# Performance work log

Measured on AMD Instinct MI355X. Metric: run time of the kernel, lower is better.

The kernel has to match this reference:

```python
import jax, jax.numpy as jnp
import numpy as np

B, L, D = 4, 4096, 256
INIT_ALPHA = -2.0
INV_TEMP = 1.0 / 0.1


def setup_inputs() -> dict:
    key = jax.random.key(0)
    k1, k2, k3, k4 = jax.random.split(key, 4)
    latents = jax.random.normal(k1, (B, L, D), dtype=jnp.float32)
    current_coords = jax.random.normal(k2, (B, L, 2), dtype=jnp.float32)
    # Linear(D, D, bias=False) weights (torch stores [out, in]; y = x @ W.T)
    lim = 1.0 / np.sqrt(D)
    Wq = jax.random.uniform(k3, (D, D), minval=-lim, maxval=lim, dtype=jnp.float32)
    Wk = jax.random.uniform(k4, (D, D), minval=-lim, maxval=lim, dtype=jnp.float32)
    alpha_raw = jnp.asarray(INIT_ALPHA, dtype=jnp.float32)
    return {"latents": latents, "current_coords": current_coords,
            "Wq": Wq, "Wk": Wk, "alpha_raw": alpha_raw, "layer_idx": 3}


def _l2norm(x, eps=1e-12):
    # F.normalize(dim=-1): x / max(||x||, eps)
    n = jnp.sqrt(jnp.sum(x * x, axis=-1, keepdims=True))
    return x / jnp.maximum(n, eps)


def reference(latents, current_coords, Wq, Wk, alpha_raw, layer_idx):
    # pred_idx selection (share_weights=True): 0 if layer_idx==0 else 1;
    # layer_idx=3 -> params given are for pred_idx=1.
    q = _l2norm(jnp.einsum('bld,ed->ble', latents, Wq))  # [B,L,D]
    k = _l2norm(jnp.einsum('bld,ed->ble', latents, Wk))  # [B,L,D]
    scores = jnp.einsum('bld,bmd->blm', q, k) * INV_TEMP  # [B,L,L]
    scores = jnp.clip(scores, -50.0, 50.0)
    W = jax.nn.softmax(scores, axis=-1)                   # [B,L,L]
    alpha = jax.nn.sigmoid(alpha_raw)
    # M = alpha*W + (1-alpha)*I; M @ coords == alpha*(W@coords) + (1-alpha)*coords
    new_coords = alpha * jnp.einsum('blm,bmc->blc', W, current_coords) \
                 + (1.0 - alpha) * current_coords
    displacement = new_coords - current_coords
    return (new_coords, displacement)
```

## Files before the change

### kernel.cpp

```cpp
#include <hip/hip_runtime.h>
#include <hip/hip_bf16.h>

#define BB 4
#define LL 4096
#define DD 256
#define MM (BB * LL)
#define NSPLIT 8
#define NQB (LL / 128)
#define KPS (LL / NSPLIT)
#define KT 64

typedef short short8 __attribute__((ext_vector_type(8)));
typedef float floatx4 __attribute__((ext_vector_type(4)));

#define SCALE_LOG2E 14.426950408889634f

__device__ __forceinline__ unsigned short f2bf(float f) {
    __hip_bfloat16 h = __float2bfloat16(f);
    union { __hip_bfloat16 h; unsigned short s; } c; c.h = h; return c.s;
}

__device__ __forceinline__ float fast_exp2(float x) {
#if __has_builtin(__builtin_amdgcn_exp2f)
    return __builtin_amdgcn_exp2f(x);
#else
    return exp2f(x);
#endif
}

__device__ __forceinline__ void stage16(const char* g, char* l, int lane) {
#if __has_builtin(__builtin_amdgcn_global_load_lds)
    __builtin_amdgcn_global_load_lds(
        (const __attribute__((address_space(1))) void*)(g + lane * 16),
        (__attribute__((address_space(3))) void*)l, 16, 0, 0);
#else
    *(short8*)(l + lane * 16) = *(const short8*)(g + lane * 16);
#endif
}

__global__ __launch_bounds__(256) void cvt_swz_kernel(
    const float* __restrict__ src, unsigned short* __restrict__ dst)
{
    const int t = blockIdx.x * 256 + threadIdx.x;
    const int r = t >> 5, c = t & 31;
    const float4 v0 = ((const float4*)src)[t * 2];
    const float4 v1 = ((const float4*)src)[t * 2 + 1];
    short8 o;
    o[0] = (short)f2bf(v0.x); o[1] = (short)f2bf(v0.y);
    o[2] = (short)f2bf(v0.z); o[3] = (short)f2bf(v0.w);
    o[4] = (short)f2bf(v1.x); o[5] = (short)f2bf(v1.y);
    o[6] = (short)f2bf(v1.z); o[7] = (short)f2bf(v1.w);
    const int cs = c ^ (r & 7);
    *(short8*)(dst + (size_t)r * DD + cs * 8) = o;
}

__global__ __launch_bounds__(256) void proj_norm_kernel(
    const float* __restrict__ latents,
    const __hip_bfloat16* __restrict__ Wq,
    const __hip_bfloat16* __restrict__ Wk,
    __hip_bfloat16* __restrict__ qn,
    __hip_bfloat16* __restrict__ kn)
{
    __shared__ char lds[KT * 512];

    const int tid  = threadIdx.x;
    const int wave = tid >> 6;
    const int lane = tid & 63;
    const int n15  = lane & 15;
    const int quad = lane >> 4;
    const int sw   = n15 & 7;

    const int pass = blockIdx.x & 1;
    const int rb   = blockIdx.x >> 1;
    const int m0   = rb * 64 + wave * 16;

    short8 afrag[8];
    const float* Abase = latents + (size_t)(m0 + n15) * DD + quad * 8;
#pragma unroll
    for (int kk = 0; kk < 8; ++kk) {
        const float4 v0 = *(const float4*)(Abase + kk * 32);
        const float4 v1 = *(const float4*)(Abase + kk * 32 + 4);
        short8 f;
        f[0] = (short)f2bf(v0.x); f[1] = (short)f2bf(v0.y);
        f[2] = (short)f2bf(v0.z); f[3] = (short)f2bf(v0.w);
        f[4] = (short)f2bf(v1.x); f[5] = (short)f2bf(v1.y);
        f[6] = (short)f2bf(v1.z); f[7] = (short)f2bf(v1.w);
        afrag[kk] = f;
    }

    const char* W = (const char*)(pass ? Wk : Wq);

    floatx4 acc[16];
#pragma unroll
    for (int ct = 0; ct < 16; ++ct) acc[ct] = (floatx4){0.f, 0.f, 0.f, 0.f};

    for (int round = 0; round < 4; ++round) {
        const char* src = W + (size_t)round * 32768 + wave * 8192;
        char* ldst = lds + wave * 8192;
#pragma unroll
        for (int j = 0; j < 8; ++j)
            stage16(src + j * 1024, ldst + j * 1024, lane);
        __syncthreads();

#pragma unroll
        for (int jt = 0; jt < 4; ++jt) {
            const int ct = round * 4 + jt;
            const char* lbase = lds + (jt * 16 + n15) * 512;
            floatx4 a = acc[ct];
#pragma unroll
            for (int kk = 0; kk < 8; ++kk) {
                const int chunk = (4 * kk + quad) ^ sw;
                short8 bfr = *(const short8*)(lbase + chunk * 16);
                a = __builtin_amdgcn_mfma_f32_16x16x32_bf16(afrag[kk], bfr, a, 0, 0, 0);
            }
            acc[ct] = a;
        }
        __syncthreads();
    }

    float ss[4] = {0.f, 0.f, 0.f, 0.f};
#pragma unroll
    for (int ct = 0; ct < 16; ++ct)
#pragma unroll
        for (int r = 0; r < 4; ++r) ss[r] += acc[ct][r] * acc[ct][r];
#pragma unroll
    for (int r = 0; r < 4; ++r) {
        ss[r] += __shfl_xor(ss[r], 1, 64);
        ss[r] += __shfl_xor(ss[r], 2, 64);
        ss[r] += __shfl_xor(ss[r], 4, 64);
        ss[r] += __shfl_xor(ss[r], 8, 64);
    }
    float sc[4];
#pragma unroll
    for (int r = 0; r < 4; ++r) {
        sc[r] = 1.f / fmaxf(sqrtf(ss[r]), 1e-12f);
        if (pass == 0) sc[r] *= SCALE_LOG2E;
    }

    if (pass == 0) {
#pragma unroll
        for (int ct = 0; ct < 16; ++ct) {
            const int col = ct * 16 + n15;
            const size_t base = (size_t)(m0 + quad * 4) * DD + col;
#pragma unroll
            for (int r = 0; r < 4; ++r)
                qn[base + (size_t)r * DD] = __float2bfloat16(acc[ct][r] * sc[r]);
        }
    } else {
#pragma unroll
        for (int ct = 0; ct < 16; ++ct) {
            const int col = ct * 16 + n15;
            const int c  = col >> 3, w8 = col & 7;
#pragma unroll
            for (int r = 0; r < 4; ++r) {
                const int row = m0 + quad * 4 + r;
                const int cs = c ^ (row & 7);
                kn[(size_t)row * DD + cs * 8 + w8] = __float2bfloat16(acc[ct][r] * sc[r]);
            }
        }
    }
}

__global__ __launch_bounds__(256) void attn_kernel(
    const __hip_bfloat16* __restrict__ qn,
    const __hip_bfloat16* __restrict__ kn,
    const float* __restrict__ coords,
    float* __restrict__ partials)
{
    __shared__ char lds[KT * 512];

    const int tid  = threadIdx.x;
    const int wave = tid >> 6;
    const int lane = tid & 63;
    const int n15  = lane & 15;
    const int quad = lane >> 4;
    const int sw   = n15 & 7;

    int bs = blockIdx.x;
    const int qb    = bs % NQB;    bs /= NQB;
    const int split = bs % NSPLIT; bs /= NSPLIT;
    const int b     = bs;

    const int mw = b * LL + qb * 128 + wave * 32;

    short8 aq[2][8];
#pragma unroll
    for (int rt = 0; rt < 2; ++rt) {
        const short* Qbase = (const short*)qn + (size_t)(mw + rt * 16 + n15) * DD + quad * 8;
#pragma unroll
        for (int kk = 0; kk < 8; ++kk)
            aq[rt][kk] = *(const short8*)(Qbase + kk * 32);
    }

    float s0[2][4], s1[2][4], s2[2][4];
#pragma unroll
    for (int rt = 0; rt < 2; ++rt)
#pragma unroll
        for (int r = 0; r < 4; ++r) { s0[rt][r] = 0.f; s1[rt][r] = 0.f; s2[rt][r] = 0.f; }

    const int key_base = b * LL + split * KPS;
    const char* ksrc = (const char*)kn + (size_t)key_base * 512;

    for (int kt = 0; kt < KPS / KT; ++kt) {
        const char* src = ksrc + (size_t)kt * KT * 512 + wave * 8192;
        char* ldst = lds + wave * 8192;
#pragma unroll
        for (int j = 0; j < 8; ++j)
            stage16(src + j * 1024, ldst + j * 1024, lane);
        __syncthreads();

#pragma unroll
        for (int ct = 0; ct < 4; ++ct) {
            const int kidx = key_base + kt * KT + ct * 16 + n15;
            const float2 cc = *(const float2*)(coords + (size_t)kidx * 2);

            floatx4 acc0 = (floatx4){0.f, 0.f, 0.f, 0.f};
            floatx4 acc1 = (floatx4){0.f, 0.f, 0.f, 0.f};
            const char* lbase = lds + (ct * 16 + n15) * 512;
#pragma unroll
            for (int kk = 0; kk < 8; ++kk) {
                const int chunk = (4 * kk + quad) ^ sw;
                short8 bfr = *(const short8*)(lbase + chunk * 16);
                acc0 = __builtin_amdgcn_mfma_f32_16x16x32_bf16(aq[0][kk], bfr, acc0, 0, 0, 0);
                acc1 = __builtin_amdgcn_mfma_f32_16x16x32_bf16(aq[1][kk], bfr, acc1, 0, 0, 0);
            }
#pragma unroll
            for (int r = 0; r < 4; ++r) {
                const float e0 = fast_exp2(acc0[r]);
                const float e1 = fast_exp2(acc1[r]);
                s0[0][r] += e0;
                s1[0][r] = fmaf(cc.x, e0, s1[0][r]);
                s2[0][r] = fmaf(cc.y, e0, s2[0][r]);
                s0[1][r] += e1;
                s1[1][r] = fmaf(cc.x, e1, s1[1][r]);
                s2[1][r] = fmaf(cc.y, e1, s2[1][r]);
            }
        }
        __syncthreads();
    }

#pragma unroll
    for (int rt = 0; rt < 2; ++rt)
#pragma unroll
        for (int r = 0; r < 4; ++r)
#pragma unroll
            for (int mask = 1; mask <= 8; mask <<= 1) {
                s0[rt][r] += __shfl_xor(s0[rt][r], mask, 64);
                s1[rt][r] += __shfl_xor(s1[rt][r], mask, 64);
                s2[rt][r] += __shfl_xor(s2[rt][r], mask, 64);
            }

    if (n15 == 0) {
#pragma unroll
        for (int rt = 0; rt < 2; ++rt)
#pragma unroll
            for (int r = 0; r < 4; ++r) {
                const int m = mw + rt * 16 + quad * 4 + r;
                float* p = partials + ((size_t)split * MM + m) * 4;
                p[0] = s0[rt][r];
                p[1] = s1[rt][r];
                p[2] = s2[rt][r];
            }
    }
}

__global__ __launch_bounds__(256) void finish_kernel(
    const float* __restrict__ partials,
    const float* __restrict__ coords,
    const float* __restrict__ alpha_raw,
    float* __restrict__ out)
{
    const int m = blockIdx.x * 256 + threadIdx.x;

    const float alpha = 1.f / (1.f + __expf(-alpha_raw[0]));

    float s0 = 0.f, s1 = 0.f, s2 = 0.f;
#pragma unroll
    for (int s = 0; s < NSPLIT; ++s) {
        const float4 v = *(const float4*)(partials + ((size_t)s * MM + m) * 4);
        s0 += v.x; s1 += v.y; s2 += v.z;
    }

    const float cx = coords[m * 2];
    const float cy = coords[m * 2 + 1];
    const float inv = 1.f / s0;
    const float nx = alpha * (s1 * inv) + (1.f - alpha) * cx;
    const float ny = alpha * (s2 * inv) + (1.f - alpha) * cy;

    out[m * 2]     = nx;
    out[m * 2 + 1] = ny;
    out[2 * MM + m * 2]     = nx - cx;
    out[2 * MM + m * 2 + 1] = ny - cy;
}

extern "C" void kernel_launch(void* const* d_in, const int* in_sizes, int n_in,
                              void* d_out, int out_size, void* d_ws, size_t ws_size,
                              hipStream_t stream) {
    const float* latents   = (const float*)d_in[0];
    const float* coords    = (const float*)d_in[1];
    const float* Wq        = (const float*)d_in[2];
    const float* Wk        = (const float*)d_in[3];
    const float* alpha_raw = (const float*)d_in[4];

    char* ws = (char*)d_ws;
    __hip_bfloat16* qn   = (__hip_bfloat16*)ws;
    __hip_bfloat16* kn   = (__hip_bfloat16*)(ws + (size_t)8 * 1024 * 1024);
    __hip_bfloat16* wq_b = (__hip_bfloat16*)(ws + (size_t)16 * 1024 * 1024);
    __hip_bfloat16* wk_b = (__hip_bfloat16*)(ws + (size_t)16 * 1024 * 1024 + 131072);
    float* partials      = (float*)(ws + (size_t)16 * 1024 * 1024 + 262144);

    float* out = (float*)d_out;

    cvt_swz_kernel<<<32, 256, 0, stream>>>(Wq, (unsigned short*)wq_b);
    cvt_swz_kernel<<<32, 256, 0, stream>>>(Wk, (unsigned short*)wk_b);
    proj_norm_kernel<<<512, 256, 0, stream>>>(latents, wq_b, wk_b, qn, kn);
    attn_kernel<<<BB * NQB * NSPLIT, 256, 0, stream>>>(qn, kn, coords, partials);
    finish_kernel<<<MM / 256, 256, 0, stream>>>(partials, coords, alpha_raw, out);
}
```

Baseline: 135.1 us.

## Double-buffer LDS staging, MFMA-fragment Q layout, LDS-staged stores, fewer key splits

Attention and projection kernels now double-buffer K/W tiles in LDS, prefetching the next tile while MFMAs consume the current one and dropping one barrier per iteration. Q is stored in a fragment-ordered layout so each lane's A fragments are contiguous 16-byte loads, and the projection writes its outputs via an LDS transpose as 16-byte vector stores instead of scattered 2-byte stores. NSPLIT drops from 8 to 4, halving the attention grid and the partials traffic. The two weight conversion launches are merged into one. Doubled LDS (64KB) lowers occupancy, and the smaller grid may underfill the GPU.

```diff
diff --git a/kernel.cpp b/kernel.cpp
--- a/kernel.cpp
+++ b/kernel.cpp
@@ -5,10 +5,11 @@
 #define LL 4096
 #define DD 256
 #define MM (BB * LL)
-#define NSPLIT 8
+#define NSPLIT 4
 #define NQB (LL / 128)
 #define KPS (LL / NSPLIT)
 #define KT 64
+#define NKT (KPS / KT)
 
 typedef short short8 __attribute__((ext_vector_type(8)));
 typedef float floatx4 __attribute__((ext_vector_type(4)));
@@ -39,9 +40,13 @@
 }
 
 __global__ __launch_bounds__(256) void cvt_swz_kernel(
-    const float* __restrict__ src, unsigned short* __restrict__ dst)
+    const float* __restrict__ srcq, const float* __restrict__ srck,
+    unsigned short* __restrict__ dstq, unsigned short* __restrict__ dstk)
 {
-    const int t = blockIdx.x * 256 + threadIdx.x;
+    const int which = blockIdx.x >> 5;
+    const float* src = which ? srck : srcq;
+    unsigned short* dst = which ? dstk : dstq;
+    const int t = (blockIdx.x & 31) * 256 + threadIdx.x;
     const int r = t >> 5, c = t & 31;
     const float4 v0 = ((const float4*)src)[t * 2];
     const float4 v1 = ((const float4*)src)[t * 2 + 1];
@@ -61,7 +66,7 @@
     __hip_bfloat16* __restrict__ qn,
     __hip_bfloat16* __restrict__ kn)
 {
-    __shared__ char lds[KT * 512];
+    __shared__ char lds[65536];
 
     const int tid  = threadIdx.x;
     const int wave = tid >> 6;
@@ -70,9 +75,10 @@
     const int quad = lane >> 4;
     const int sw   = n15 & 7;
 
-    const int pass = blockIdx.x & 1;
-    const int rb   = blockIdx.x >> 1;
-    const int m0   = rb * 64 + wave * 16;
+    const int pass  = blockIdx.x & 1;
+    const int rbase = (blockIdx.x >> 1) * 64;
+    const int m0    = rbase + wave * 16;
+    const int r160  = rbase >> 4;
 
     short8 afrag[8];
     const float* Abase = latents + (size_t)(m0 + n15) * DD + quad * 8;
@@ -94,18 +100,26 @@
 #pragma unroll
     for (int ct = 0; ct < 16; ++ct) acc[ct] = (floatx4){0.f, 0.f, 0.f, 0.f};
 
+    {
+        const char* src = W + wave * 8192;
+        char* dst = lds + wave * 8192;
+#pragma unroll
+        for (int j = 0; j < 8; ++j) stage16(src + j * 1024, dst + j * 1024, lane);
+    }
+
     for (int round = 0; round < 4; ++round) {
-        const char* src = W + (size_t)round * 32768 + wave * 8192;
-        char* ldst = lds + wave * 8192;
-#pragma unroll
-        for (int j = 0; j < 8; ++j)
-            stage16(src + j * 1024, ldst + j * 1024, lane);
         __syncthreads();
-
+        if (round + 1 < 4) {
+            const char* src = W + (size_t)(round + 1) * 32768 + wave * 8192;
+            char* dst = lds + ((round + 1) & 1) * 32768 + wave * 8192;
+#pragma unroll
+            for (int j = 0; j < 8; ++j) stage16(src + j * 1024, dst + j * 1024, lane);
+        }
+        const char* buf = lds + (round & 1) * 32768;
 #pragma unroll
         for (int jt = 0; jt < 4; ++jt) {
             const int ct = round * 4 + jt;
-            const char* lbase = lds + (jt * 16 + n15) * 512;
+            const char* lbase = buf + (jt * 16 + n15) * 512;
             floatx4 a = acc[ct];
 #pragma unroll
             for (int kk = 0; kk < 8; ++kk) {
@@ -115,7 +129,6 @@
             }
             acc[ct] = a;
         }
-        __syncthreads();
     }
 
     float ss[4] = {0.f, 0.f, 0.f, 0.f};
@@ -137,25 +150,40 @@
         if (pass == 0) sc[r] *= SCALE_LOG2E;
     }
 
-    if (pass == 0) {
-#pragma unroll
-        for (int ct = 0; ct < 16; ++ct) {
-            const int col = ct * 16 + n15;
-            const size_t base = (size_t)(m0 + quad * 4) * DD + col;
-#pragma unroll
-            for (int r = 0; r < 4; ++r)
-                qn[base + (size_t)r * DD] = __float2bfloat16(acc[ct][r] * sc[r]);
-        }
-    } else {
-#pragma unroll
-        for (int ct = 0; ct < 16; ++ct) {
-            const int col = ct * 16 + n15;
-            const int c  = col >> 3, w8 = col & 7;
+    unsigned short* tb = (unsigned short*)lds;
+#pragma unroll
+    for (int h = 0; h < 2; ++h) {
+        __syncthreads();
+#pragma unroll
+        for (int cth = 0; cth < 8; ++cth) {
+            const int ct = h * 8 + cth;
+            const int col = cth * 16 + n15;
 #pragma unroll
             for (int r = 0; r < 4; ++r) {
-                const int row = m0 + quad * 4 + r;
-                const int cs = c ^ (row & 7);
-                kn[(size_t)row * DD + cs * 8 + w8] = __float2bfloat16(acc[ct][r] * sc[r]);
+                const int rl = wave * 16 + quad * 4 + r;
+                tb[rl * 136 + col] = f2bf(acc[ct][r] * sc[r]);
+            }
+        }
+        __syncthreads();
+        if (pass == 0) {
+#pragma unroll
+            for (int j = 0; j < 4; ++j) {
+                const int g = tid + j * 256;
+                const int n15r = g & 15, q2 = (g >> 4) & 3, kkh = (g >> 6) & 3, r16l = (g >> 8) & 3;
+                const int rl = r16l * 16 + n15r;
+                short8 v = *(const short8*)(tb + rl * 136 + kkh * 32 + q2 * 8);
+                const size_t chunk = (((size_t)(r160 + r16l) * 8 + (h * 4 + kkh)) * 4 + q2) * 16 + n15r;
+                *(short8*)((char*)qn + chunk * 16) = v;
+            }
+        } else {
+#pragma unroll
+            for (int j = 0; j < 4; ++j) {
+                const int g = tid + j * 256;
+                const int csl = g & 15, rl = g >> 4;
+                const int row = rbase + rl;
+                const int ci = csl ^ (row & 7);
+                short8 v = *(const short8*)(tb + rl * 136 + ci * 8);
+                *(short8*)((char*)kn + (size_t)row * 512 + (h * 16 + csl) * 16) = v;
             }
         }
     }
@@ -167,7 +195,7 @@
     const float* __restrict__ coords,
     float* __restrict__ partials)
 {
-    __shared__ char lds[KT * 512];
+    __shared__ char lds[2 * 32768];
 
     const int tid  = threadIdx.x;
     const int wave = tid >> 6;
@@ -183,31 +211,41 @@
 
     const int mw = b * LL + qb * 128 + wave * 32;
 
-    short8 aq[2][8];
-#pragma unroll
-    for (int rt = 0; rt < 2; ++rt) {
-        const short* Qbase = (const short*)qn + (size_t)(mw + rt * 16 + n15) * DD + quad * 8;
-#pragma unroll
-        for (int kk = 0; kk < 8; ++kk)
-            aq[rt][kk] = *(const short8*)(Qbase + kk * 32);
-    }
-
-    float s0[2][4], s1[2][4], s2[2][4];
-#pragma unroll
-    for (int rt = 0; rt < 2; ++rt)
-#pragma unroll
-        for (int r = 0; r < 4; ++r) { s0[rt][r] = 0.f; s1[rt][r] = 0.f; s2[rt][r] = 0.f; }
-
     const int key_base = b * LL + split * KPS;
     const char* ksrc = (const char*)kn + (size_t)key_base * 512;
 
-    for (int kt = 0; kt < KPS / KT; ++kt) {
-        const char* src = ksrc + (size_t)kt * KT * 512 + wave * 8192;
-        char* ldst = lds + wave * 8192;
-#pragma unroll
-        for (int j = 0; j < 8; ++j)
-            stage16(src + j * 1024, ldst + j * 1024, lane);
+    {
+        const char* src = ksrc + wave * 8192;
+        char* dst = lds + wave * 8192;
+#pragma unroll
+        for (int j = 0; j < 8; ++j) stage16(src + j * 1024, dst + j * 1024, lane);
+    }
+
+    short8 aq[2][8];
+    const int t16 = mw >> 4;
+#pragma unroll
+    for (int rt = 0; rt < 2; ++rt)
+#pragma unroll
+        for (int kk = 0; kk < 8; ++kk) {
+            const size_t chunk = (((size_t)(t16 + rt) * 8 + kk) * 4 + quad) * 16 + n15;
+            aq[rt][kk] = *(const short8*)((const char*)qn + chunk * 16);
+        }
+
+    float s0[2][4], s1[2][4], s2[2][4];
+#pragma unroll
+    for (int rt = 0; rt < 2; ++rt)
+#pragma unroll
+        for (int r = 0; r < 4; ++r) { s0[rt][r] = 0.f; s1[rt][r] = 0.f; s2[rt][r] = 0.f; }
+
+    for (int kt = 0; kt < NKT; ++kt) {
         __syncthreads();
+        if (kt + 1 < NKT) {
+            const char* src = ksrc + (size_t)(kt + 1) * KT * 512 + wave * 8192;
+            char* dst = lds + ((kt + 1) & 1) * 32768 + wave * 8192;
+#pragma unroll
+            for (int j = 0; j < 8; ++j) stage16(src + j * 1024, dst + j * 1024, lane);
+        }
+        const char* buf = lds + (kt & 1) * 32768;
 
 #pragma unroll
         for (int ct = 0; ct < 4; ++ct) {
@@ -216,7 +254,7 @@
 
             floatx4 acc0 = (floatx4){0.f, 0.f, 0.f, 0.f};
             floatx4 acc1 = (floatx4){0.f, 0.f, 0.f, 0.f};
-            const char* lbase = lds + (ct * 16 + n15) * 512;
+            const char* lbase = buf + (ct * 16 + n15) * 512;
 #pragma unroll
             for (int kk = 0; kk < 8; ++kk) {
                 const int chunk = (4 * kk + quad) ^ sw;
@@ -236,7 +274,6 @@
                 s2[1][r] = fmaf(cc.y, e1, s2[1][r]);
             }
         }
-        __syncthreads();
     }
 
 #pragma unroll
@@ -311,8 +348,7 @@
 
     float* out = (float*)d_out;
 
-    cvt_swz_kernel<<<32, 256, 0, stream>>>(Wq, (unsigned short*)wq_b);
-    cvt_swz_kernel<<<32, 256, 0, stream>>>(Wk, (unsigned short*)wk_b);
+    cvt_swz_kernel<<<64, 256, 0, stream>>>(Wq, Wk, (unsigned short*)wq_b, (unsigned short*)wk_b);
     proj_norm_kernel<<<512, 256, 0, stream>>>(latents, wq_b, wk_b, qn, kn);
     attn_kernel<<<BB * NQB * NSPLIT, 256, 0, stream>>>(qn, kn, coords, partials);
     finish_kernel<<<MM / 256, 256, 0, stream>>>(partials, coords, alpha_raw, out);
```

After: 124.9 us. -7.5%, faster.
